# Performance work log

Hardware: AMD Instinct MI355X
Metric: run time of the kernel (lower is better)

The kernel has to match this reference:

```python
import jax, jax.numpy as jnp
import numpy as np

B, IN, H = 4096, 1024, 1024


def setup_inputs() -> dict:
    key = jax.random.key(0)
    k1, k2, k3, k4 = jax.random.split(key, 4)
    x = jax.random.normal(k1, (B, IN), dtype=jnp.float32)
    h_prev = jax.random.normal(k2, (B, H), dtype=jnp.float32)
    c_prev = jax.random.normal(k3, (B, H), dtype=jnp.float32)
    # Kaiming-uniform-ish init for W: bound = sqrt(6 / fan_in)
    fan_in = IN + H
    bound = np.sqrt(6.0 / fan_in)
    W = jax.random.uniform(k4, (4 * H, IN + H), dtype=jnp.float32,
                           minval=-bound, maxval=bound)
    # bias zero except forget-gate bias = 1.0 (first H entries)
    b = jnp.zeros((4 * H,), dtype=jnp.float32).at[:H].set(1.0)
    return {"x": x, "h_prev": h_prev, "c_prev": c_prev, "W": W, "b": b}


def reference(x, h_prev, c_prev, W, b):
    Hdim = c_prev.shape[1]
    combined = jnp.concatenate([x, h_prev], axis=1)        # (B, IN+H)
    gates = combined @ W.T + b                             # (B, 4H)
    f = jax.nn.sigmoid(gates[:, :Hdim])
    i = jax.nn.sigmoid(gates[:, Hdim:2 * Hdim])
    g = jnp.tanh(gates[:, 2 * Hdim:3 * Hdim])
    o = jax.nn.sigmoid(gates[:, 3 * Hdim:])
    c_t = f * c_prev + i * g
    h_t = o * jnp.tanh(c_t)
    return (h_t, c_t)
```

## Files before the change

### kernel.cpp

```cpp
#include <hip/hip_runtime.h>
#include <stdint.h>

#define Bn 4096
#define INn 1024
#define Hn 1024
#define Kn 2048
#define Nn 4096

#define BM 128
#define BN 256
#define BK 64
#define KT (Kn / BK)

typedef __attribute__((ext_vector_type(8))) short bf16x8;
typedef __attribute__((ext_vector_type(4))) float f32x4;
typedef __attribute__((ext_vector_type(4))) unsigned short us4;

__device__ __forceinline__ unsigned short f2bf(float f) {
  uint32_t u = __float_as_uint(f);
  u += 0x7fffu + ((u >> 16) & 1u);
  return (unsigned short)(u >> 16);
}

typedef __attribute__((address_space(3))) unsigned int as3_uint;
typedef const __attribute__((address_space(1))) unsigned int as1_uint;

__device__ __forceinline__ void gload16(const unsigned short* g, unsigned short* l) {
  __builtin_amdgcn_global_load_lds((as1_uint*)g, (as3_uint*)l, 16, 0, 0);
}

__device__ __forceinline__ float sigm(float x) { return 1.f / (1.f + __expf(-x)); }
__device__ __forceinline__ float tanh_fast(float x) { return 2.f / (1.f + __expf(-2.f * x)) - 1.f; }

__global__ void pack_all(const float* __restrict__ x, const float* __restrict__ h,
                         const float* __restrict__ W,
                         unsigned short* __restrict__ Abf, unsigned short* __restrict__ Wbf) {
  const long XQ = (long)Bn * INn / 4;
  const long WQ = (long)Nn * Kn / 4;
  const long total = XQ + XQ + WQ;
  const long stride = (long)gridDim.x * blockDim.x;
  for (long q = (long)blockIdx.x * blockDim.x + threadIdx.x; q < total; q += stride) {
    float4 v;
    unsigned short* dst;
    if (q < XQ) {
      long e = q << 2;
      v = *(const float4*)(x + e);
      dst = Abf + ((long)(e >> 10) * Kn) + (e & 1023);
    } else if (q < 2 * XQ) {
      long e = (q - XQ) << 2;
      v = *(const float4*)(h + e);
      dst = Abf + ((long)(e >> 10) * Kn) + INn + (e & 1023);
    } else {
      long e = (q - 2 * XQ) << 2;
      v = *(const float4*)(W + e);
      dst = Wbf + e;
    }
    us4 o;
    o.x = f2bf(v.x); o.y = f2bf(v.y); o.z = f2bf(v.z); o.w = f2bf(v.w);
    *(us4*)dst = o;
  }
}

#define STAGE_A(t_, b_) do {                                                     \
    const int k0_ = (t_) * BK;                                                   \
    gload16(Ag + (long)(brow + srow) * Kn + k0_ + scol,                          \
            &bufA[b_][srow * BK + sc8 * 8]);                                     \
    gload16(Ag + (long)(brow + 64 + srow) * Kn + k0_ + scol,                     \
            &bufA[b_][(64 + srow) * BK + sc8 * 8]);                              \
  } while (0)
#define STAGE_B(t_, b_, j_) do {                                                 \
    const int k0_ = (t_) * BK;                                                   \
    const int rb_ = (j_) * 64 + srow;                                            \
    const int grow_ = ((rb_ >> 4) & 3) * Hn + h0 + ((rb_ >> 6) << 4) + (rb_ & 15);\
    gload16(Wg + (long)grow_ * Kn + k0_ + scol,                                  \
            &bufB[b_][rb_ * BK + sc8 * 8]);                                      \
  } while (0)
#define FENCE() do { asm volatile("" ::: "memory"); __builtin_amdgcn_sched_barrier(0); } while (0)

__global__ void __launch_bounds__(512, 2)
lstm_gemm_fused(const unsigned short* __restrict__ Ag,
                const unsigned short* __restrict__ Wg,
                const float* __restrict__ c_prev,
                const float* __restrict__ bias,
                float* __restrict__ out) {
  __shared__ unsigned short bufA[3][BM * BK];
  __shared__ unsigned short bufB[3][BN * BK];

  const int tid = threadIdx.x;
  const int lane = tid & 63;
  const int wid = tid >> 6;
  const int wr = wid >> 2;
  const int wc = wid & 3;
  const int brow = blockIdx.y * BM;
  const int h0 = blockIdx.x * 64;

  const int srow = tid >> 3;
  const int sc8 = tid & 7;
  const int scol = ((sc8 ^ (srow & 7)) * 8);

  const int l15 = lane & 15;
  const int s7 = l15 & 7;
  const int cA = lane >> 4;
  const int aOff0 = (wr * 64 + l15) * BK + ((cA) ^ s7) * 8;
  const int aOff1 = (wr * 64 + l15) * BK + ((cA + 4) ^ s7) * 8;
  const int bOff0 = (wc * 64 + l15) * BK + ((cA) ^ s7) * 8;
  const int bOff1 = (wc * 64 + l15) * BK + ((cA + 4) ^ s7) * 8;

  f32x4 acc[4][4] = {};

  STAGE_A(0, 0); STAGE_B(0, 0, 0); STAGE_B(0, 0, 1); STAGE_B(0, 0, 2); STAGE_B(0, 0, 3);
  STAGE_A(1, 1); STAGE_B(1, 1, 0); STAGE_B(1, 1, 1); STAGE_B(1, 1, 2); STAGE_B(1, 1, 3);

  for (int t = 0; t < KT; ++t) {
    const int bi = t % 3;
    const int sb = (t + 2) % 3;
    if (t < KT - 1) asm volatile("s_waitcnt vmcnt(6)" ::: "memory");
    else            asm volatile("s_waitcnt vmcnt(0)" ::: "memory");
    __builtin_amdgcn_s_barrier();
    FENCE();

    if (t + 2 < KT) {
      STAGE_A(t + 2, sb);
      STAGE_B(t + 2, sb, 0); STAGE_B(t + 2, sb, 1);
      STAGE_B(t + 2, sb, 2); STAGE_B(t + 2, sb, 3);
    }

    const unsigned short* As = bufA[bi];
    const unsigned short* Bs = bufB[bi];
    bf16x8 af[4][2], bfr[4][2];
#pragma unroll
    for (int n = 0; n < 4; ++n) {
      bfr[n][0] = *(const bf16x8*)&Bs[bOff0 + n * 16 * BK];
      bfr[n][1] = *(const bf16x8*)&Bs[bOff1 + n * 16 * BK];
    }
#pragma unroll
    for (int m = 0; m < 4; ++m) {
      af[m][0] = *(const bf16x8*)&As[aOff0 + m * 16 * BK];
      af[m][1] = *(const bf16x8*)&As[aOff1 + m * 16 * BK];
    }
    __builtin_amdgcn_s_setprio(1);
#pragma unroll
    for (int m = 0; m < 4; ++m)
#pragma unroll
      for (int n = 0; n < 4; ++n) {
        acc[m][n] = __builtin_amdgcn_mfma_f32_16x16x32_bf16(af[m][0], bfr[n][0], acc[m][n], 0, 0, 0);
        acc[m][n] = __builtin_amdgcn_mfma_f32_16x16x32_bf16(af[m][1], bfr[n][1], acc[m][n], 0, 0, 0);
      }
    __builtin_amdgcn_s_setprio(0);
    FENCE();
  }

  const int hcol = h0 + wc * 16 + l15;
  const float bf_ = bias[hcol];
  const float bi_ = bias[Hn + hcol];
  const float bg_ = bias[2 * Hn + hcol];
  const float bo_ = bias[3 * Hn + hcol];
  const int rbase = brow + wr * 64 + ((lane >> 4) << 2);
  const long BH = (long)Bn * Hn;
#pragma unroll
  for (int m = 0; m < 4; ++m) {
#pragma unroll
    for (int j = 0; j < 4; ++j) {
      const long r = rbase + m * 16 + j;
      const float f = sigm(acc[m][0][j] + bf_);
      const float i_ = sigm(acc[m][1][j] + bi_);
      const float g = tanh_fast(acc[m][2][j] + bg_);
      const float o = sigm(acc[m][3][j] + bo_);
      const float cp = c_prev[r * Hn + hcol];
      const float ct = f * cp + i_ * g;
      out[r * Hn + hcol] = o * tanh_fast(ct);
      out[BH + r * Hn + hcol] = ct;
    }
  }
}

extern "C" void kernel_launch(void* const* d_in, const int* in_sizes, int n_in,
                              void* d_out, int out_size, void* d_ws, size_t ws_size,
                              hipStream_t stream) {
  const float* x      = (const float*)d_in[0];
  const float* h_prev = (const float*)d_in[1];
  const float* c_prev = (const float*)d_in[2];
  const float* W      = (const float*)d_in[3];
  const float* bias   = (const float*)d_in[4];
  float* out = (float*)d_out;

  unsigned short* Abf = (unsigned short*)d_ws;
  unsigned short* Wbf = Abf + (long)Bn * Kn;

  pack_all<<<2048, 256, 0, stream>>>(x, h_prev, W, Abf, Wbf);

  dim3 grid(Hn / 64, Bn / BM);
  lstm_gemm_fused<<<grid, 512, 0, stream>>>(Abf, Wbf, c_prev, bias, out);
}
```

Baseline: 215.5 us.

## Enlarge GEMM tile to 256x256 with 4x2 warp layout and double buffering

Doubles the block's row tile from 128 to 256 and changes the wave layout to 4x2, so each wave computes a 64x128 output sub-tile (32 accumulators) instead of 64x64. This raises arithmetic intensity per LDS fragment load. The triple-buffered LDS pipeline becomes a double buffer with a full vmcnt(0) wait each step, to keep LDS within budget. Fragment loads are split into two K halves to limit register pressure. Risks: higher VGPR use may reduce occupancy under launch_bounds(512,2), less load/compute overlap, and only half as many blocks (256 on the grid).

```diff
diff --git a/kernel.cpp b/kernel.cpp
--- a/kernel.cpp
+++ b/kernel.cpp
@@ -7,7 +7,7 @@
 #define Kn 2048
 #define Nn 4096
 
-#define BM 128
+#define BM 256
 #define BN 256
 #define BK 64
 #define KT (Kn / BK)
@@ -61,19 +61,19 @@
   }
 }
 
-#define STAGE_A(t_, b_) do {                                                     \
-    const int k0_ = (t_) * BK;                                                   \
-    gload16(Ag + (long)(brow + srow) * Kn + k0_ + scol,                          \
-            &bufA[b_][srow * BK + sc8 * 8]);                                     \
-    gload16(Ag + (long)(brow + 64 + srow) * Kn + k0_ + scol,                     \
-            &bufA[b_][(64 + srow) * BK + sc8 * 8]);                              \
+#define STAGE_A(t_, b_) do {                                                      \
+    const int k0_ = (t_) * BK;                                                    \
+    gload16(Ag + (long)(brow + srow      ) * Kn + k0_ + scol, &bufA[b_][(srow      ) * BK + sc8 * 8]); \
+    gload16(Ag + (long)(brow + srow + 64 ) * Kn + k0_ + scol, &bufA[b_][(srow + 64 ) * BK + sc8 * 8]); \
+    gload16(Ag + (long)(brow + srow + 128) * Kn + k0_ + scol, &bufA[b_][(srow + 128) * BK + sc8 * 8]); \
+    gload16(Ag + (long)(brow + srow + 192) * Kn + k0_ + scol, &bufA[b_][(srow + 192) * BK + sc8 * 8]); \
   } while (0)
-#define STAGE_B(t_, b_, j_) do {                                                 \
-    const int k0_ = (t_) * BK;                                                   \
-    const int rb_ = (j_) * 64 + srow;                                            \
-    const int grow_ = ((rb_ >> 4) & 3) * Hn + h0 + ((rb_ >> 6) << 4) + (rb_ & 15);\
-    gload16(Wg + (long)grow_ * Kn + k0_ + scol,                                  \
-            &bufB[b_][rb_ * BK + sc8 * 8]);                                      \
+#define STAGE_B(t_, b_) do {                                                      \
+    const int k0_ = (t_) * BK;                                                    \
+    gload16(Wg + (long)(g0     ) * Kn + k0_ + scol, &bufB[b_][(srow      ) * BK + sc8 * 8]); \
+    gload16(Wg + (long)(g0 + 16) * Kn + k0_ + scol, &bufB[b_][(srow + 64 ) * BK + sc8 * 8]); \
+    gload16(Wg + (long)(g0 + 32) * Kn + k0_ + scol, &bufB[b_][(srow + 128) * BK + sc8 * 8]); \
+    gload16(Wg + (long)(g0 + 48) * Kn + k0_ + scol, &bufB[b_][(srow + 192) * BK + sc8 * 8]); \
   } while (0)
 #define FENCE() do { asm volatile("" ::: "memory"); __builtin_amdgcn_sched_barrier(0); } while (0)
 
@@ -83,78 +83,80 @@
                 const float* __restrict__ c_prev,
                 const float* __restrict__ bias,
                 float* __restrict__ out) {
-  __shared__ unsigned short bufA[3][BM * BK];
-  __shared__ unsigned short bufB[3][BN * BK];
+  __shared__ unsigned short bufA[2][BM * BK];
+  __shared__ unsigned short bufB[2][BN * BK];
 
   const int tid = threadIdx.x;
   const int lane = tid & 63;
   const int wid = tid >> 6;
-  const int wr = wid >> 2;
-  const int wc = wid & 3;
+  const int wr = wid >> 1;
+  const int wc = wid & 1;
   const int brow = blockIdx.y * BM;
   const int h0 = blockIdx.x * 64;
 
   const int srow = tid >> 3;
   const int sc8 = tid & 7;
   const int scol = ((sc8 ^ (srow & 7)) * 8);
+  const int g0 = ((srow >> 4) & 3) * Hn + h0 + (srow & 15);
 
   const int l15 = lane & 15;
   const int s7 = l15 & 7;
   const int cA = lane >> 4;
   const int aOff0 = (wr * 64 + l15) * BK + ((cA) ^ s7) * 8;
   const int aOff1 = (wr * 64 + l15) * BK + ((cA + 4) ^ s7) * 8;
-  const int bOff0 = (wc * 64 + l15) * BK + ((cA) ^ s7) * 8;
-  const int bOff1 = (wc * 64 + l15) * BK + ((cA + 4) ^ s7) * 8;
-
-  f32x4 acc[4][4] = {};
-
-  STAGE_A(0, 0); STAGE_B(0, 0, 0); STAGE_B(0, 0, 1); STAGE_B(0, 0, 2); STAGE_B(0, 0, 3);
-  STAGE_A(1, 1); STAGE_B(1, 1, 0); STAGE_B(1, 1, 1); STAGE_B(1, 1, 2); STAGE_B(1, 1, 3);
+  const int bOff0 = (wc * 128 + l15) * BK + ((cA) ^ s7) * 8;
+  const int bOff1 = (wc * 128 + l15) * BK + ((cA + 4) ^ s7) * 8;
+
+  f32x4 acc[4][8] = {};
+
+  STAGE_A(0, 0); STAGE_B(0, 0);
 
   for (int t = 0; t < KT; ++t) {
-    const int bi = t % 3;
-    const int sb = (t + 2) % 3;
-    if (t < KT - 1) asm volatile("s_waitcnt vmcnt(6)" ::: "memory");
-    else            asm volatile("s_waitcnt vmcnt(0)" ::: "memory");
+    asm volatile("s_waitcnt vmcnt(0)" ::: "memory");
     __builtin_amdgcn_s_barrier();
     FENCE();
 
-    if (t + 2 < KT) {
-      STAGE_A(t + 2, sb);
-      STAGE_B(t + 2, sb, 0); STAGE_B(t + 2, sb, 1);
-      STAGE_B(t + 2, sb, 2); STAGE_B(t + 2, sb, 3);
+    if (t + 1 < KT) {
+      const int nb = (t + 1) & 1;
+      STAGE_A(t + 1, nb); STAGE_B(t + 1, nb);
     }
 
-    const unsigned short* As = bufA[bi];
-    const unsigned short* Bs = bufB[bi];
-    bf16x8 af[4][2], bfr[4][2];
-#pragma unroll
-    for (int n = 0; n < 4; ++n) {
-      bfr[n][0] = *(const bf16x8*)&Bs[bOff0 + n * 16 * BK];
-      bfr[n][1] = *(const bf16x8*)&Bs[bOff1 + n * 16 * BK];
-    }
-#pragma unroll
-    for (int m = 0; m < 4; ++m) {
-      af[m][0] = *(const bf16x8*)&As[aOff0 + m * 16 * BK];
-      af[m][1] = *(const bf16x8*)&As[aOff1 + m * 16 * BK];
-    }
+    const unsigned short* As = bufA[t & 1];
+    const unsigned short* Bs = bufB[t & 1];
+    bf16x8 af[4], bfr[8];
+
+#pragma unroll
+    for (int n = 0; n < 8; ++n) bfr[n] = *(const bf16x8*)&Bs[bOff0 + n * 16 * BK];
+#pragma unroll
+    for (int m = 0; m < 4; ++m) af[m] = *(const bf16x8*)&As[aOff0 + m * 16 * BK];
     __builtin_amdgcn_s_setprio(1);
 #pragma unroll
     for (int m = 0; m < 4; ++m)
 #pragma unroll
-      for (int n = 0; n < 4; ++n) {
-        acc[m][n] = __builtin_amdgcn_mfma_f32_16x16x32_bf16(af[m][0], bfr[n][0], acc[m][n], 0, 0, 0);
-        acc[m][n] = __builtin_amdgcn_mfma_f32_16x16x32_bf16(af[m][1], bfr[n][1], acc[m][n], 0, 0, 0);
-      }
+      for (int n = 0; n < 8; ++n)
+        acc[m][n] = __builtin_amdgcn_mfma_f32_16x16x32_bf16(af[m], bfr[n], acc[m][n], 0, 0, 0);
+    __builtin_amdgcn_s_setprio(0);
+
+#pragma unroll
+    for (int n = 0; n < 8; ++n) bfr[n] = *(const bf16x8*)&Bs[bOff1 + n * 16 * BK];
+#pragma unroll
+    for (int m = 0; m < 4; ++m) af[m] = *(const bf16x8*)&As[aOff1 + m * 16 * BK];
+    __builtin_amdgcn_s_setprio(1);
+#pragma unroll
+    for (int m = 0; m < 4; ++m)
+#pragma unroll
+      for (int n = 0; n < 8; ++n)
+        acc[m][n] = __builtin_amdgcn_mfma_f32_16x16x32_bf16(af[m], bfr[n], acc[m][n], 0, 0, 0);
     __builtin_amdgcn_s_setprio(0);
     FENCE();
   }
 
-  const int hcol = h0 + wc * 16 + l15;
-  const float bf_ = bias[hcol];
-  const float bi_ = bias[Hn + hcol];
-  const float bg_ = bias[2 * Hn + hcol];
-  const float bo_ = bias[3 * Hn + hcol];
+  const int hq0 = h0 + wc * 32 + l15;
+  const int hq1 = hq0 + 16;
+  const float bF0 = bias[hq0],        bF1 = bias[hq1];
+  const float bI0 = bias[Hn + hq0],   bI1 = bias[Hn + hq1];
+  const float bG0 = bias[2*Hn + hq0], bG1 = bias[2*Hn + hq1];
+  const float bO0 = bias[3*Hn + hq0], bO1 = bias[3*Hn + hq1];
   const int rbase = brow + wr * 64 + ((lane >> 4) << 2);
   const long BH = (long)Bn * Hn;
 #pragma unroll
@@ -162,14 +164,26 @@
 #pragma unroll
     for (int j = 0; j < 4; ++j) {
       const long r = rbase + m * 16 + j;
-      const float f = sigm(acc[m][0][j] + bf_);
-      const float i_ = sigm(acc[m][1][j] + bi_);
-      const float g = tanh_fast(acc[m][2][j] + bg_);
-      const float o = sigm(acc[m][3][j] + bo_);
-      const float cp = c_prev[r * Hn + hcol];
-      const float ct = f * cp + i_ * g;
-      out[r * Hn + hcol] = o * tanh_fast(ct);
-      out[BH + r * Hn + hcol] = ct;
+      {
+        const float f = sigm(acc[m][0][j] + bF0);
+        const float i_ = sigm(acc[m][1][j] + bI0);
+        const float g = tanh_fast(acc[m][2][j] + bG0);
+        const float o = sigm(acc[m][3][j] + bO0);
+        const float cp = c_prev[r * Hn + hq0];
+        const float ct = f * cp + i_ * g;
+        out[r * Hn + hq0] = o * tanh_fast(ct);
+        out[BH + r * Hn + hq0] = ct;
+      }
+      {
+        const float f = sigm(acc[m][4][j] + bF1);
+        const float i_ = sigm(acc[m][5][j] + bI1);
+        const float g = tanh_fast(acc[m][6][j] + bG1);
+        const float o = sigm(acc[m][7][j] + bO1);
+        const float cp = c_prev[r * Hn + hq1];
+        const float ct = f * cp + i_ * g;
+        out[r * Hn + hq1] = o * tanh_fast(ct);
+        out[BH + r * Hn + hq1] = ct;
+      }
     }
   }
 }
```

Result: faster. 202.2 us (-6.2%).

## Interleave LDS fragment loads and global staging with MFMA sub-blocks in GEMM loop

Applied to the files above, without the earlier changes.

Splits each K-tile iteration into four MFMA phases, each covering half the M rows for one K half. Each phase is overlapped with LDS fragment loads for the next phase and with part of the global-to-LDS staging. The next tile's first fragments are prefetched before the last MFMA phase, and the wait/barrier point is moved accordingly. The goal is to hide LDS read latency and the issue cost of global loads behind matrix-core work, at the price of four barriers per iteration instead of one and more live fragment registers.

```diff
diff --git a/kernel.cpp b/kernel.cpp
--- a/kernel.cpp
+++ b/kernel.cpp
@@ -76,6 +76,13 @@
             &bufB[b_][rb_ * BK + sc8 * 8]);                                      \
   } while (0)
 #define FENCE() do { asm volatile("" ::: "memory"); __builtin_amdgcn_sched_barrier(0); } while (0)
+#define MFMA8(ml, ap, bs) do {                                                   \
+    _Pragma("unroll")                                                            \
+    for (int n = 0; n < 4; ++n) {                                                \
+      acc[(ml)][n]     = __builtin_amdgcn_mfma_f32_16x16x32_bf16(ap[0], bs[n], acc[(ml)][n], 0, 0, 0);     \
+      acc[(ml) + 1][n] = __builtin_amdgcn_mfma_f32_16x16x32_bf16(ap[1], bs[n], acc[(ml) + 1][n], 0, 0, 0); \
+    }                                                                            \
+  } while (0)
 
 __global__ void __launch_bounds__(512, 2)
 lstm_gemm_fused(const unsigned short* __restrict__ Ag,
@@ -107,46 +114,73 @@
   const int bOff1 = (wc * 64 + l15) * BK + ((cA + 4) ^ s7) * 8;
 
   f32x4 acc[4][4] = {};
+  bf16x8 a01k0[2], a23k0[2], a01k1[2], a23k1[2], bk0[4], bk1[4];
 
   STAGE_A(0, 0); STAGE_B(0, 0, 0); STAGE_B(0, 0, 1); STAGE_B(0, 0, 2); STAGE_B(0, 0, 3);
   STAGE_A(1, 1); STAGE_B(1, 1, 0); STAGE_B(1, 1, 1); STAGE_B(1, 1, 2); STAGE_B(1, 1, 3);
+  asm volatile("s_waitcnt vmcnt(6)" ::: "memory");
+  __builtin_amdgcn_s_barrier();
+  FENCE();
+  {
+    const unsigned short* As = bufA[0];
+    const unsigned short* Bs = bufB[0];
+    a01k0[0] = *(const bf16x8*)&As[aOff0];
+    a01k0[1] = *(const bf16x8*)&As[aOff0 + 16 * BK];
+#pragma unroll
+    for (int n = 0; n < 4; ++n) bk0[n] = *(const bf16x8*)&Bs[bOff0 + n * 16 * BK];
+  }
 
   for (int t = 0; t < KT; ++t) {
     const int bi = t % 3;
     const int sb = (t + 2) % 3;
-    if (t < KT - 1) asm volatile("s_waitcnt vmcnt(6)" ::: "memory");
-    else            asm volatile("s_waitcnt vmcnt(0)" ::: "memory");
-    __builtin_amdgcn_s_barrier();
-    FENCE();
-
-    if (t + 2 < KT) {
-      STAGE_A(t + 2, sb);
-      STAGE_B(t + 2, sb, 0); STAGE_B(t + 2, sb, 1);
-      STAGE_B(t + 2, sb, 2); STAGE_B(t + 2, sb, 3);
-    }
-
+    const int bn = (t + 1) % 3;
+    const bool st = (t + 2) < KT;
     const unsigned short* As = bufA[bi];
     const unsigned short* Bs = bufB[bi];
-    bf16x8 af[4][2], bfr[4][2];
-#pragma unroll
-    for (int n = 0; n < 4; ++n) {
-      bfr[n][0] = *(const bf16x8*)&Bs[bOff0 + n * 16 * BK];
-      bfr[n][1] = *(const bf16x8*)&Bs[bOff1 + n * 16 * BK];
+
+    if (st) STAGE_A(t + 2, sb);
+    a23k0[0] = *(const bf16x8*)&As[aOff0 + 32 * BK];
+    a23k0[1] = *(const bf16x8*)&As[aOff0 + 48 * BK];
+    __builtin_amdgcn_s_setprio(1);
+    MFMA8(0, a01k0, bk0);
+    __builtin_amdgcn_s_setprio(0);
+    __builtin_amdgcn_s_barrier();
+    FENCE();
+
+    if (st) { STAGE_B(t + 2, sb, 0); STAGE_B(t + 2, sb, 1); }
+    a01k1[0] = *(const bf16x8*)&As[aOff1];
+    a01k1[1] = *(const bf16x8*)&As[aOff1 + 16 * BK];
+#pragma unroll
+    for (int n = 0; n < 4; ++n) bk1[n] = *(const bf16x8*)&Bs[bOff1 + n * 16 * BK];
+    __builtin_amdgcn_s_setprio(1);
+    MFMA8(2, a23k0, bk0);
+    __builtin_amdgcn_s_setprio(0);
+    __builtin_amdgcn_s_barrier();
+    FENCE();
+
+    if (st) { STAGE_B(t + 2, sb, 2); STAGE_B(t + 2, sb, 3); }
+    a23k1[0] = *(const bf16x8*)&As[aOff1 + 32 * BK];
+    a23k1[1] = *(const bf16x8*)&As[aOff1 + 48 * BK];
+    __builtin_amdgcn_s_setprio(1);
+    MFMA8(0, a01k1, bk1);
+    __builtin_amdgcn_s_setprio(0);
+    if (t < KT - 2) asm volatile("s_waitcnt vmcnt(6)" ::: "memory");
+    else            asm volatile("s_waitcnt vmcnt(0)" ::: "memory");
+    __builtin_amdgcn_s_barrier();
+    FENCE();
+
+    if (t + 1 < KT) {
+      const unsigned short* An = bufA[bn];
+      const unsigned short* Bsn = bufB[bn];
+      a01k0[0] = *(const bf16x8*)&An[aOff0];
+      a01k0[1] = *(const bf16x8*)&An[aOff0 + 16 * BK];
+#pragma unroll
+      for (int n = 0; n < 4; ++n) bk0[n] = *(const bf16x8*)&Bsn[bOff0 + n * 16 * BK];
     }
-#pragma unroll
-    for (int m = 0; m < 4; ++m) {
-      af[m][0] = *(const bf16x8*)&As[aOff0 + m * 16 * BK];
-      af[m][1] = *(const bf16x8*)&As[aOff1 + m * 16 * BK];
-    }
-    __builtin_amdgcn_s_setprio(1);
-#pragma unroll
-    for (int m = 0; m < 4; ++m)
-#pragma unroll
-      for (int n = 0; n < 4; ++n) {
-        acc[m][n] = __builtin_amdgcn_mfma_f32_16x16x32_bf16(af[m][0], bfr[n][0], acc[m][n], 0, 0, 0);
-        acc[m][n] = __builtin_amdgcn_mfma_f32_16x16x32_bf16(af[m][1], bfr[n][1], acc[m][n], 0, 0, 0);
-      }
-    __builtin_amdgcn_s_setprio(0);
+    __builtin_amdgcn_s_setprio(1);
+    MFMA8(2, a23k1, bk1);
+    __builtin_amdgcn_s_setprio(0);
+    __builtin_amdgcn_s_barrier();
     FENCE();
   }
 
```

Result: slower. 245.1 us (+13.7%).
